# Kernel optimization log

Hardware: AMD Instinct MI355X
Metric: run time of the kernel (lower is better)

The kernel has to match this reference:

```python
import jax, jax.numpy as jnp
import numpy as np


def setup_inputs() -> dict:
    key = jax.random.key(0)
    k1, k2 = jax.random.split(key)
    x = jax.random.normal(k1, (16, 2048, 256), dtype=jnp.float32)
    embed = jax.random.normal(k2, (1024, 256), dtype=jnp.float32)
    return {"x": x, "embed": embed}


def reference(x, embed):
    shape = x.shape
    xf = x.reshape(-1, shape[-1])  # (N, d)
    dist = -(jnp.sum(xf * xf, axis=1, keepdims=True)
             - 2.0 * (xf @ embed.T)
             + jnp.sum(embed * embed, axis=1)[None, :])  # (N, K)
    embed_ind = jnp.argmax(dist, axis=-1)  # (N,)
    embed_ind = embed_ind.reshape(shape[:-1])  # (B, T)
    quantize = embed[embed_ind]  # (B, T, d) gather
    return quantize, embed_ind
```

## Files before the change

### kernel.cpp

```cpp
#include <hip/hip_runtime.h>
#include <stdint.h>

#define NROWS 32768
#define DIMS  256
#define KCB   1024
#define BM 128
#define BN 128
#define GY (KCB/BN)
#define MARGIN 0.25f
#define CROWS 16

typedef _Float16 half8   __attribute__((ext_vector_type(8)));
typedef float    f32x4   __attribute__((ext_vector_type(4)));
typedef short    short4v __attribute__((ext_vector_type(4)));
typedef short    short8v __attribute__((ext_vector_type(8)));

__device__ __forceinline__ void gload_lds16(const void* g, void* l) {
    __builtin_amdgcn_global_load_lds(
        (const __attribute__((address_space(1))) uint32_t*)g,
        (__attribute__((address_space(3))) uint32_t*)l, 16, 0, 0);
}

__device__ __forceinline__ short f16h(float v) {
    _Float16 hh = (_Float16)v;
    return __builtin_bit_cast(short, hh);
}

__global__ __launch_bounds__(256) void split_all(
    const float* __restrict__ x, short* __restrict__ Xh,
    const float* __restrict__ embed, short* __restrict__ Eh,
    float* __restrict__ he2)
{
    if (blockIdx.x < 4096) {
        int T = blockIdx.x * 256 + threadIdx.x;
        int l = T & 63, c = (T >> 6) & 7, G = T >> 9;
        int row = G * 16 + (l & 15);
        int kb  = c * 32 + (l >> 4) * 8;
        const f32x4* src = (const f32x4*)(x + (size_t)row * DIMS + kb);
        f32x4 a = src[0], b = src[1];
        short8v h;
        #pragma unroll
        for (int e = 0; e < 4; ++e) { h[e] = f16h(a[e]); h[4 + e] = f16h(b[e]); }
        *(short8v*)(Xh + (size_t)G * 4096 + c * 512 + l * 8) = h;
    } else {
        int r = (blockIdx.x - 4096) * 4 + (threadIdx.x >> 6);
        int l = threadIdx.x & 63;
        f32x4 v = ((const f32x4*)(embed + (size_t)r * DIMS))[l];
        float s = v[0]*v[0] + v[1]*v[1] + v[2]*v[2] + v[3]*v[3];
        #pragma unroll
        for (int off = 32; off > 0; off >>= 1) s += __shfl_down(s, off, 64);
        if (l == 0) he2[r] = 0.5f * s;
        int G = r >> 4, cc = l >> 3;
        int fl = (r & 15) + 16 * ((l >> 1) & 3);
        size_t base = (size_t)G * 4096 + cc * 512 + fl * 8 + (l & 1) * 4;
        short4v h;
        #pragma unroll
        for (int e = 0; e < 4; ++e) h[e] = f16h(v[e]);
        *(short4v*)(Eh + base) = h;
    }
}

__global__ __launch_bounds__(256, 4) void vq_mfma(
    const short* __restrict__ Xh, const short* __restrict__ Eh,
    const float* __restrict__ he2, float4* __restrict__ part)
{
    __shared__ char lds[32768];

    const int t = threadIdx.x, lane = t & 63, w = t >> 6;
    const int wm = w >> 1, wn = w & 1;
    const int lhi = lane >> 4, c15 = lane & 15;
    const int sid = blockIdx.x;
    const int xcd = sid & 7, j = sid >> 3;
    const int rb = xcd * 32 + (j >> 3), cb = j & 7;
    const int rowBase = rb * BM, colBase = cb * BN;

    const char* gA[4];
    const char* gB[4];
    #pragma unroll
    for (int m = 0; m < 4; ++m)
        gA[m] = (const char*)Xh + (size_t)(rb * 8 + wm * 4 + m) * 8192 + lane * 16;
    #pragma unroll
    for (int n = 0; n < 4; ++n)
        gB[n] = (const char*)Eh + (size_t)(cb * 8 + wn * 4 + n) * 8192 + lane * 16;
    char* lw = lds + w * 8192;

    f32x4 acc[4][4];
    #pragma unroll
    for (int m = 0; m < 4; ++m)
        #pragma unroll
        for (int n = 0; n < 4; ++n) acc[m][n] = (f32x4){0.f, 0.f, 0.f, 0.f};

    #pragma unroll
    for (int m = 0; m < 4; ++m) gload_lds16(gA[m], lw + m * 1024);
    #pragma unroll
    for (int n = 0; n < 4; ++n) gload_lds16(gB[n], lw + 4096 + n * 1024);

    #pragma unroll
    for (int c = 0; c < 8; ++c) {
        asm volatile("s_waitcnt vmcnt(0)" ::: "memory");
        __builtin_amdgcn_sched_barrier(0);

        half8 A[4], B[4];
        #pragma unroll
        for (int m = 0; m < 4; ++m)
            A[m] = *(const half8*)(lw + m * 1024 + lane * 16);
        #pragma unroll
        for (int n = 0; n < 4; ++n)
            B[n] = *(const half8*)(lw + 4096 + n * 1024 + lane * 16);
        asm volatile("s_waitcnt lgkmcnt(0)" ::: "memory");
        __builtin_amdgcn_sched_barrier(0);

        if (c < 7) {
            #pragma unroll
            for (int m = 0; m < 4; ++m)
                gload_lds16(gA[m] + (c + 1) * 1024, lw + m * 1024);
            #pragma unroll
            for (int n = 0; n < 4; ++n)
                gload_lds16(gB[n] + (c + 1) * 1024, lw + 4096 + n * 1024);
        }
        __builtin_amdgcn_sched_barrier(0);

        __builtin_amdgcn_s_setprio(1);
        #pragma unroll
        for (int m = 0; m < 4; ++m)
            #pragma unroll
            for (int n = 0; n < 4; ++n)
                acc[m][n] = __builtin_amdgcn_mfma_f32_16x16x32_f16(A[m], B[n], acc[m][n], 0, 0, 0);
        __builtin_amdgcn_s_setprio(0);
    }

    __syncthreads();
    float* S1 = (float*)lds;
    int*   I1 = (int*)(lds + 8704);
    float* S2 = (float*)(lds + 17408);

    float h2[4];
    #pragma unroll
    for (int n = 0; n < 4; ++n) h2[n] = he2[colBase + 64 * wn + 16 * n + c15];
    const int colg0 = colBase + 64 * wn + c15;

    #pragma unroll
    for (int m = 0; m < 4; ++m) {
        #pragma unroll
        for (int reg = 0; reg < 4; ++reg) {
            float b1 = acc[m][0][reg] - h2[0];
            int   i1 = colg0;
            float b2 = -3.4e38f;
            #pragma unroll
            for (int n = 1; n < 4; ++n) {
                float s = acc[m][n][reg] - h2[n];
                if (s > b1) { b2 = b1; b1 = s; i1 = colg0 + 16 * n; }
                else        { b2 = fmaxf(b2, s); }
            }
            {
                float ob1 = __shfl_xor(b1, 1, 64);
                int   oi1 = __shfl_xor(i1, 1, 64);
                float ob2 = __shfl_xor(b2, 1, 64);
                if (ob1 > b1 || (ob1 == b1 && oi1 < i1)) {
                    b2 = fmaxf(b1, ob2); b1 = ob1; i1 = oi1;
                } else {
                    b2 = fmaxf(b2, ob1);
                }
            }
            if ((c15 & 1) == 0) {
                int row  = 64 * wm + 16 * m + 4 * lhi + reg;
                int slot = wn * 8 + (c15 >> 1);
                S1[row * 17 + slot] = b1;
                I1[row * 17 + slot] = i1;
                S2[row * 17 + slot] = b2;
            }
        }
    }
    __syncthreads();

    if (t < BM) {
        float b1 = S1[t * 17]; int i1 = I1[t * 17]; float b2 = S2[t * 17];
        #pragma unroll
        for (int s = 1; s < 16; ++s) {
            float c1 = S1[t * 17 + s]; int j1 = I1[t * 17 + s];
            float c2 = S2[t * 17 + s];
            if (c1 > b1 || (c1 == b1 && j1 < i1)) { b2 = fmaxf(b1, c2); b1 = c1; i1 = j1; }
            else                                  { b2 = fmaxf(b2, c1); }
        }
        part[(size_t)(rowBase + t) * GY + cb] =
            make_float4(b1, __int_as_float(i1), b2, 0.f);
    }
}

__device__ __forceinline__ float dot16(f32x4 xa, f32x4 xb, f32x4 xc, f32x4 xd,
                                       const float* __restrict__ erow, int q) {
    const f32x4* er = (const f32x4*)(erow + q * 16);
    f32x4 ea = er[0], eb = er[1], ec = er[2], ed = er[3];
    float s = xa[0] * ea[0];
    s = fmaf(xa[1], ea[1], s); s = fmaf(xa[2], ea[2], s); s = fmaf(xa[3], ea[3], s);
    s = fmaf(xb[0], eb[0], s); s = fmaf(xb[1], eb[1], s);
    s = fmaf(xb[2], eb[2], s); s = fmaf(xb[3], eb[3], s);
    s = fmaf(xc[0], ec[0], s); s = fmaf(xc[1], ec[1], s);
    s = fmaf(xc[2], ec[2], s); s = fmaf(xc[3], ec[3], s);
    s = fmaf(xd[0], ed[0], s); s = fmaf(xd[1], ed[1], s);
    s = fmaf(xd[2], ed[2], s); s = fmaf(xd[3], ed[3], s);
    s += __shfl_xor(s, 1, 64);
    s += __shfl_xor(s, 2, 64);
    s += __shfl_xor(s, 4, 64);
    s += __shfl_xor(s, 8, 64);
    return s;
}

__global__ __launch_bounds__(256) void vq_combine(
    const float4* __restrict__ part, const float* __restrict__ embed,
    const float* __restrict__ x, const float* __restrict__ he2,
    float* __restrict__ outq, float* __restrict__ outi)
{
    __shared__ int idxS[CROWS];
    __shared__ int flagL[CROWS];
    __shared__ int flagN;
    const int t = threadIdx.x, l = t & 63, w = t >> 6;
    const int rowBase = blockIdx.x * CROWS;

    if (t == 0) flagN = 0;
    __syncthreads();

    if (t < CROWS) {
        const int row = rowBase + t;
        float4 p = part[(size_t)row * GY];
        float b1 = p.x; int i1 = __float_as_int(p.y); float b2 = p.z;
        #pragma unroll
        for (int g = 1; g < GY; ++g) {
            float4 q = part[(size_t)row * GY + g];
            float c1 = q.x; int j1 = __float_as_int(q.y); float c2 = q.z;
            if (c1 > b1 || (c1 == b1 && j1 < i1)) { b2 = fmaxf(b1, c2); b1 = c1; i1 = j1; }
            else                                  { b2 = fmaxf(b2, c1); }
        }
        idxS[t] = i1;
        outi[row] = (float)i1;
        if (b1 - b2 < MARGIN) {
            int s = atomicAdd(&flagN, 1);
            flagL[s] = t;
        }
    }
    __syncthreads();

    #pragma unroll
    for (int qq = 0; qq < (CROWS * 64) / 256; ++qq) {
        int f = t + 256 * qq;
        int r = f >> 6, c4 = f & 63;
        int e = idxS[r];
        f32x4 v = *(const f32x4*)(embed + (size_t)e * DIMS + c4 * 4);
        *(f32x4*)(outq + (size_t)(rowBase + r) * DIMS + c4 * 4) = v;
    }
    __syncthreads();

    const int nf = flagN;
    const int q = l & 15, pgrp = l >> 4;
    for (int it = w; it < nf; it += 4) {
        int rrow = rowBase + flagL[it];
        const f32x4* xr = (const f32x4*)(x + (size_t)rrow * DIMS + q * 16);
        f32x4 xa = xr[0], xb = xr[1], xc = xr[2], xd = xr[3];

        float4 pc[GY];
        #pragma unroll
        for (int g = 0; g < GY; ++g) pc[g] = part[(size_t)rrow * GY + g];
        float B1 = pc[0].x;
        #pragma unroll
        for (int g = 1; g < GY; ++g) B1 = fmaxf(B1, pc[g].x);
        const float T = B1 - MARGIN;

        float wb = -3.4e38f; int wi = 0x7fffffff;
        #pragma unroll
        for (int g = 0; g < GY; ++g) {
            if (pc[g].z >= T) {
                #pragma unroll 2
                for (int i = 0; i < BN / 4; ++i) {
                    int code = g * BN + i * 4 + pgrp;
                    float s = dot16(xa, xb, xc, xd,
                                    embed + (size_t)code * DIMS, q) - he2[code];
                    if (s > wb || (s == wb && code < wi)) { wb = s; wi = code; }
                }
            } else if (pc[g].x >= T) {
                int code = __float_as_int(pc[g].y);
                float s = dot16(xa, xb, xc, xd,
                                embed + (size_t)code * DIMS, q) - he2[code];
                if (s > wb || (s == wb && code < wi)) { wb = s; wi = code; }
            }
        }
        #pragma unroll
        for (int msk = 16; msk <= 32; msk <<= 1) {
            float ob = __shfl_xor(wb, msk, 64);
            int   oi = __shfl_xor(wi, msk, 64);
            if (ob > wb || (ob == wb && oi < wi)) { wb = ob; wi = oi; }
        }
        f32x4 v = ((const f32x4*)(embed + (size_t)wi * DIMS))[l];
        ((f32x4*)(outq + (size_t)rrow * DIMS))[l] = v;
        if (l == 0) outi[rrow] = (float)wi;
    }
}

extern "C" void kernel_launch(void* const* d_in, const int* in_sizes, int n_in,
                              void* d_out, int out_size, void* d_ws, size_t ws_size,
                              hipStream_t stream) {
    const float* x     = (const float*)d_in[0];
    const float* embed = (const float*)d_in[1];
    char* ws = (char*)d_ws;
    float*  he2  = (float*)ws;
    float4* part = (float4*)(ws + 8192);
    short*  Xh   = (short*)(ws + 8192 + 4194304);
    short*  Eh   = (short*)(ws + 8192 + 4194304 + 16777216);
    float*  out  = (float*)d_out;
    float*  outi = out + (size_t)NROWS * DIMS;

    split_all<<<4352, 256, 0, stream>>>(x, Xh, embed, Eh, he2);
    vq_mfma<<<(NROWS / BM) * GY, 256, 0, stream>>>(Xh, Eh, he2, part);
    vq_combine<<<NROWS / CROWS, 256, 0, stream>>>(part, embed, x, he2, out, outi);
}
```

Before: 71.77 us.

## Fuse combine stage into MFMA kernel using last-block-per-panel atomic counter

Removes the separate vq_combine launch. Each vq_mfma block now bumps an atomic counter for its row panel, and the last of the GY column blocks for that panel merges the partial argmax results. That block also writes the gathered codewords and indices and re-checks ambiguous rows in fp32. This drops one kernel launch and its tail, at the cost of a memset, threadfences, and a heavier, serialized epilogue in the last block of each panel. It may also raise register pressure in the MFMA kernel.

Result: slower. 184.9 us (+157.6%).

```diff
diff --git a/kernel.cpp b/kernel.cpp
--- a/kernel.cpp
+++ b/kernel.cpp
@@ -8,7 +8,6 @@
 #define BN 128
 #define GY (KCB/BN)
 #define MARGIN 0.25f
-#define CROWS 16
 
 typedef _Float16 half8   __attribute__((ext_vector_type(8)));
 typedef float    f32x4   __attribute__((ext_vector_type(4)));
@@ -60,11 +59,37 @@
     }
 }
 
+__device__ __forceinline__ float dot16(f32x4 xa, f32x4 xb, f32x4 xc, f32x4 xd,
+                                       const float* __restrict__ erow, int q) {
+    const f32x4* er = (const f32x4*)(erow + q * 16);
+    f32x4 ea = er[0], eb = er[1], ec = er[2], ed = er[3];
+    float s = xa[0] * ea[0];
+    s = fmaf(xa[1], ea[1], s); s = fmaf(xa[2], ea[2], s); s = fmaf(xa[3], ea[3], s);
+    s = fmaf(xb[0], eb[0], s); s = fmaf(xb[1], eb[1], s);
+    s = fmaf(xb[2], eb[2], s); s = fmaf(xb[3], eb[3], s);
+    s = fmaf(xc[0], ec[0], s); s = fmaf(xc[1], ec[1], s);
+    s = fmaf(xc[2], ec[2], s); s = fmaf(xc[3], ec[3], s);
+    s = fmaf(xd[0], ed[0], s); s = fmaf(xd[1], ed[1], s);
+    s = fmaf(xd[2], ed[2], s); s = fmaf(xd[3], ed[3], s);
+    s += __shfl_xor(s, 1, 64);
+    s += __shfl_xor(s, 2, 64);
+    s += __shfl_xor(s, 4, 64);
+    s += __shfl_xor(s, 8, 64);
+    return s;
+}
+
 __global__ __launch_bounds__(256, 4) void vq_mfma(
     const short* __restrict__ Xh, const short* __restrict__ Eh,
-    const float* __restrict__ he2, float4* __restrict__ part)
+    const float* __restrict__ he2, float4* __restrict__ part,
+    const float* __restrict__ x, const float* __restrict__ embed,
+    float* __restrict__ outq, float* __restrict__ outi,
+    int* __restrict__ panelCnt)
 {
     __shared__ char lds[32768];
+    __shared__ int  idxS[BM];
+    __shared__ int  flagL[BM];
+    __shared__ int  flagN;
+    __shared__ int  lastFlag;
 
     const int t = threadIdx.x, lane = t & 63, w = t >> 6;
     const int wm = w >> 1, wn = w & 1;
@@ -185,42 +210,20 @@
         part[(size_t)(rowBase + t) * GY + cb] =
             make_float4(b1, __int_as_float(i1), b2, 0.f);
     }
-}
-
-__device__ __forceinline__ float dot16(f32x4 xa, f32x4 xb, f32x4 xc, f32x4 xd,
-                                       const float* __restrict__ erow, int q) {
-    const f32x4* er = (const f32x4*)(erow + q * 16);
-    f32x4 ea = er[0], eb = er[1], ec = er[2], ed = er[3];
-    float s = xa[0] * ea[0];
-    s = fmaf(xa[1], ea[1], s); s = fmaf(xa[2], ea[2], s); s = fmaf(xa[3], ea[3], s);
-    s = fmaf(xb[0], eb[0], s); s = fmaf(xb[1], eb[1], s);
-    s = fmaf(xb[2], eb[2], s); s = fmaf(xb[3], eb[3], s);
-    s = fmaf(xc[0], ec[0], s); s = fmaf(xc[1], ec[1], s);
-    s = fmaf(xc[2], ec[2], s); s = fmaf(xc[3], ec[3], s);
-    s = fmaf(xd[0], ed[0], s); s = fmaf(xd[1], ed[1], s);
-    s = fmaf(xd[2], ed[2], s); s = fmaf(xd[3], ed[3], s);
-    s += __shfl_xor(s, 1, 64);
-    s += __shfl_xor(s, 2, 64);
-    s += __shfl_xor(s, 4, 64);
-    s += __shfl_xor(s, 8, 64);
-    return s;
-}
-
-__global__ __launch_bounds__(256) void vq_combine(
-    const float4* __restrict__ part, const float* __restrict__ embed,
-    const float* __restrict__ x, const float* __restrict__ he2,
-    float* __restrict__ outq, float* __restrict__ outi)
-{
-    __shared__ int idxS[CROWS];
-    __shared__ int flagL[CROWS];
-    __shared__ int flagN;
-    const int t = threadIdx.x, l = t & 63, w = t >> 6;
-    const int rowBase = blockIdx.x * CROWS;
+
+    __syncthreads();
+    if (t == 0) {
+        __threadfence();
+        int old = atomicAdd(&panelCnt[rb], 1);
+        lastFlag = (old == GY - 1);
+    }
+    __syncthreads();
+    if (!lastFlag) return;
+    __threadfence();
 
     if (t == 0) flagN = 0;
     __syncthreads();
-
-    if (t < CROWS) {
+    if (t < BM) {
         const int row = rowBase + t;
         float4 p = part[(size_t)row * GY];
         float b1 = p.x; int i1 = __float_as_int(p.y); float b2 = p.z;
@@ -241,7 +244,7 @@
     __syncthreads();
 
     #pragma unroll
-    for (int qq = 0; qq < (CROWS * 64) / 256; ++qq) {
+    for (int qq = 0; qq < (BM * 64) / 256; ++qq) {
         int f = t + 256 * qq;
         int r = f >> 6, c4 = f & 63;
         int e = idxS[r];
@@ -251,7 +254,7 @@
     __syncthreads();
 
     const int nf = flagN;
-    const int q = l & 15, pgrp = l >> 4;
+    const int q = c15, pgrp = lhi;
     for (int it = w; it < nf; it += 4) {
         int rrow = rowBase + flagL[it];
         const f32x4* xr = (const f32x4*)(x + (size_t)rrow * DIMS + q * 16);
@@ -289,9 +292,9 @@
             int   oi = __shfl_xor(wi, msk, 64);
             if (ob > wb || (ob == wb && oi < wi)) { wb = ob; wi = oi; }
         }
-        f32x4 v = ((const f32x4*)(embed + (size_t)wi * DIMS))[l];
-        ((f32x4*)(outq + (size_t)rrow * DIMS))[l] = v;
-        if (l == 0) outi[rrow] = (float)wi;
+        f32x4 v = ((const f32x4*)(embed + (size_t)wi * DIMS))[lane];
+        ((f32x4*)(outq + (size_t)rrow * DIMS))[lane] = v;
+        if (lane == 0) outi[rrow] = (float)wi;
     }
 }
 
@@ -301,14 +304,16 @@
     const float* x     = (const float*)d_in[0];
     const float* embed = (const float*)d_in[1];
     char* ws = (char*)d_ws;
-    float*  he2  = (float*)ws;
-    float4* part = (float4*)(ws + 8192);
-    short*  Xh   = (short*)(ws + 8192 + 4194304);
-    short*  Eh   = (short*)(ws + 8192 + 4194304 + 16777216);
+    float*  he2      = (float*)ws;
+    int*    panelCnt = (int*)(ws + 4096);
+    float4* part     = (float4*)(ws + 8192);
+    short*  Xh       = (short*)(ws + 8192 + 4194304);
+    short*  Eh       = (short*)(ws + 8192 + 4194304 + 16777216);
     float*  out  = (float*)d_out;
     float*  outi = out + (size_t)NROWS * DIMS;
 
+    hipMemsetAsync(panelCnt, 0, 256 * sizeof(int), stream);
     split_all<<<4352, 256, 0, stream>>>(x, Xh, embed, Eh, he2);
-    vq_mfma<<<(NROWS / BM) * GY, 256, 0, stream>>>(Xh, Eh, he2, part);
-    vq_combine<<<NROWS / CROWS, 256, 0, stream>>>(part, embed, x, he2, out, outi);
-}
+    vq_mfma<<<(NROWS / BM) * GY, 256, 0, stream>>>(Xh, Eh, he2, part,
+                                                   x, embed, out, outi, panelCnt);
+}
```
